# Kernel optimization log

Measured on AMD Instinct MI355X. Metric: run time of the kernel, lower is better.

Reference implementation:

```python
import jax, jax.numpy as jnp
import numpy as np

N = 100000
DEG = 16            # edges per source node (1 self-loop + 15 random)
E = N * DEG
IN_F = 128
OUT_F = 64
ALPHA = 0.2         # leaky relu negative slope


def _build_edges(key):
    # edges sorted by src (as adj.nonzero() would be), every node has >=1 out-edge
    src = jnp.repeat(jnp.arange(N, dtype=jnp.int32), DEG)
    dst = jax.random.randint(key, (E,), 0, N, dtype=jnp.int32)
    # force a self-loop as the first edge of every block
    self_pos = jnp.arange(E, dtype=jnp.int32) % DEG == 0
    dst = jnp.where(self_pos, src, dst)
    return jnp.stack([src, dst])  # [2, E]


def setup_inputs() -> dict:
    key = jax.random.key(0)
    k1, k2, k3, k4, k5, k6 = jax.random.split(key, 6)
    return {
        "input": jax.random.normal(k1, (N, IN_F), dtype=jnp.float32),
        "edge": _build_edges(k2),
        "W_high": jax.random.normal(k3, (IN_F, OUT_F), dtype=jnp.float32) * 0.1,
        "W_low": jax.random.normal(k4, (IN_F, OUT_F), dtype=jnp.float32) * 0.1,
        "a_high": jax.random.normal(k5, (1, 2 * OUT_F), dtype=jnp.float32) * 0.1,
        "a_low": jax.random.normal(k6, (1, 2 * OUT_F), dtype=jnp.float32) * 0.1,
    }


def _relu6(x):
    return jnp.clip(x, 0.0, 6.0)


def reference(input, edge, W_high, W_low, a_high, a_low):
    n = input.shape[0]
    src, dst = edge[0], edge[1]

    h_high = input @ W_high          # [N, F]
    h_low = input @ W_low            # [N, F]

    # a.mm(cat(h[src], h[dst]).T) == (h @ a_src)[src] + (h @ a_dst)[dst]
    f = W_high.shape[1]
    s_high = (h_high @ a_high[0, :f])[src] + (h_high @ a_high[0, f:])[dst]  # [E]
    s_low = (h_low @ a_low[0, :f])[src] + (h_low @ a_low[0, f:])[dst]

    edge_e_high = jnp.exp(-jax.nn.leaky_relu(s_high, ALPHA))  # [E], > 0
    edge_e_low = jnp.exp(-jax.nn.leaky_relu(s_low, ALPHA))

    seg = lambda v: jax.ops.segment_sum(v, src, num_segments=n, indices_are_sorted=True)

    # rowsum uses RAW exp values (before relu6/dropout), matching the source
    e_high_rowsum = seg(edge_e_high)[:, None]  # [N, 1]
    e_low_rowsum = seg(edge_e_low)[:, None]

    # relu6 clamp (dropout p=0 -> identity, eval mode)
    eh = _relu6(edge_e_high)
    el = _relu6(edge_e_low)

    # m @ (h[src] +/- h[dst]) == segment_sum over src of per-edge features
    h_agg_high = seg(h_high[src] + h_high[dst])   # [N, F]
    h_agg_low = seg(h_low[src] - h_low[dst])      # [N, F]

    # spmm: out[i] = sum_{(i,j)} e_ij * h_agg[j]
    h_prime_high = seg(eh[:, None] * h_agg_high[dst]) / e_high_rowsum
    h_prime_low = seg(el[:, None] * h_agg_low[dst]) / e_low_rowsum

    h_prime = 0.5 * (h_prime_high + h_prime_low)
    return _relu6(h_prime)  # concat=True
```

## Files before the change

### kernel.cpp

```cpp
#include <hip/hip_runtime.h>

#define N_NODES 100000
#define DEG 16
#define IN_F 128
#define OUT_F 64
#define E_EDGES (N_NODES * DEG)

typedef __bf16 bf16x8 __attribute__((ext_vector_type(8)));
typedef unsigned short u16x8 __attribute__((ext_vector_type(8)));
typedef float f32x4 __attribute__((ext_vector_type(4)));
typedef unsigned int u32x4 __attribute__((ext_vector_type(4)));

union BF8 { u16x8 u; bf16x8 b; };

__device__ inline float lo_bf(unsigned int u) {
    union { unsigned int i; float f; } v; v.i = u << 16; return v.f;
}
__device__ inline float hi_bf(unsigned int u) {
    union { unsigned int i; float f; } v; v.i = u & 0xFFFF0000u; return v.f;
}
__device__ inline unsigned short f2bf(float f) {
    union { float f; unsigned int i; } v; v.f = f;
    return (unsigned short)((v.i + 0x7FFFu + ((v.i >> 16) & 1u)) >> 16);
}
__device__ inline unsigned int packbf(float a, float b) {
    return (unsigned int)f2bf(a) | ((unsigned int)f2bf(b) << 16);
}

__global__ __launch_bounds__(256) void k_gemm(
    const float* __restrict__ in, const float* __restrict__ Wh,
    const float* __restrict__ Wl, unsigned int* __restrict__ H)
{
    __shared__ __align__(16) unsigned short ldsW[2][64][136];
    __shared__ __align__(16) unsigned short ldsA[64][136];

    {
        int n  = threadIdx.x & 63;
        int kg = threadIdx.x >> 6;
        #pragma unroll
        for (int m = 0; m < 2; m++) {
            const float* W = m ? Wl : Wh;
            #pragma unroll
            for (int i = 0; i < 32; i += 2) {
                int k = kg * 32 + i;
                float a = W[k * 64 + n];
                float b = W[(k + 1) * 64 + n];
                *(unsigned int*)&ldsW[m][n][k] = packbf(a, b);
            }
        }
    }

    int row0B = blockIdx.x * 64;
    {
        const f32x4* src = (const f32x4*)(in + (size_t)row0B * IN_F);
        #pragma unroll
        for (int i = 0; i < 8; i++) {
            int cch = threadIdx.x + 256 * i;
            int row = cch >> 5;
            int kc = (cch & 31) * 4;
            int grow = row0B + row;
            f32x4 v = (grow < N_NODES) ? src[cch]
                      : *(const f32x4*)(in + (size_t)(N_NODES - 1) * IN_F + kc);
            unsigned int p0 = packbf(v[0], v[1]);
            unsigned int p1 = packbf(v[2], v[3]);
            *(unsigned int*)&ldsA[row][kc]     = p0;
            *(unsigned int*)&ldsA[row][kc + 2] = p1;
        }
    }
    __syncthreads();

    int wv = threadIdx.x >> 6;
    int lane = threadIdx.x & 63;
    int quad = lane >> 4, c = lane & 15;
    int row0 = row0B + wv * 16;

    bf16x8 afrag[4];
    #pragma unroll
    for (int kb = 0; kb < 4; kb++) {
        BF8 a;
        a.u = *(const u16x8*)&ldsA[wv * 16 + c][kb * 32 + quad * 8];
        afrag[kb] = a.b;
    }

    f32x4 acc[2][4];
    #pragma unroll
    for (int m = 0; m < 2; m++)
        #pragma unroll
        for (int t = 0; t < 4; t++) acc[m][t] = (f32x4){0, 0, 0, 0};

    #pragma unroll
    for (int kb = 0; kb < 4; kb++) {
        #pragma unroll
        for (int t = 0; t < 4; t++) {
            int n = t * 16 + c;
            BF8 bh, bl;
            bh.u = *(const u16x8*)&ldsW[0][n][kb * 32 + quad * 8];
            bl.u = *(const u16x8*)&ldsW[1][n][kb * 32 + quad * 8];
            acc[0][t] = __builtin_amdgcn_mfma_f32_16x16x32_bf16(afrag[kb], bh.b, acc[0][t], 0, 0, 0);
            acc[1][t] = __builtin_amdgcn_mfma_f32_16x16x32_bf16(afrag[kb], bl.b, acc[1][t], 0, 0, 0);
        }
    }

    #pragma unroll
    for (int r = 0; r < 4; r++) {
        int row = row0 + quad * 4 + r;
        if (row >= N_NODES) continue;
        size_t base = (size_t)row * OUT_F + c;
        #pragma unroll
        for (int t = 0; t < 4; t++)
            H[base + t * 16] = packbf(acc[0][t][r], acc[1][t][r]);
    }
}

__global__ __launch_bounds__(256) void k_agg(
    const unsigned int* __restrict__ H, const int* __restrict__ dst,
    const float* __restrict__ ah, const float* __restrict__ al,
    unsigned int* __restrict__ HAGG, f32x4* __restrict__ s)
{
    int lane = threadIdx.x & 63;
    int node = __builtin_amdgcn_readfirstlane(blockIdx.x * 4 + (threadIdx.x >> 6));
    const int* dp = dst + node * DEG;

    unsigned int hu = H[(size_t)node * 64 + lane];
    float hh = lo_bf(hu);
    float hl = hi_bf(hu);
    float sh = 16.0f * hh;
    float sl = 16.0f * hl;

    #pragma unroll
    for (int half = 0; half < 2; half++) {
        unsigned int u[8];
        #pragma unroll
        for (int t = 0; t < 8; t++) {
            int j = dp[half * 8 + t];
            u[t] = H[(size_t)j * 64 + lane];
        }
        #pragma unroll
        for (int t = 0; t < 8; t++) { sh += lo_bf(u[t]); sl -= hi_bf(u[t]); }
    }
    HAGG[(size_t)node * 64 + lane] = packbf(sh, sl);

    float ph = hh * ah[lane];
    float qh = hh * ah[64 + lane];
    float pl = hl * al[lane];
    float ql = hl * al[64 + lane];
    #pragma unroll
    for (int o = 32; o > 0; o >>= 1) {
        ph += __shfl_xor(ph, o);
        qh += __shfl_xor(qh, o);
        pl += __shfl_xor(pl, o);
        ql += __shfl_xor(ql, o);
    }
    if (lane == 0) s[node] = (f32x4){ph, qh, pl, ql};
}

__global__ __launch_bounds__(256) void k_out(
    const unsigned int* __restrict__ HAGG, const int* __restrict__ dst,
    const f32x4* __restrict__ s, float* __restrict__ out)
{
    int lane = threadIdx.x & 63;
    int node = __builtin_amdgcn_readfirstlane(blockIdx.x * 4 + (threadIdx.x >> 6));
    const int* dp = dst + node * DEG;

    int jl = dp[lane & 15];
    f32x4 si = s[node];
    f32x4 sj = s[jl];
    float xh = si.x + sj.y;
    float xl = si.z + sj.w;
    float lh = xh > 0.0f ? xh : 0.2f * xh;
    float ll = xl > 0.0f ? xl : 0.2f * xl;
    float wh = __expf(-lh);
    float wl = __expf(-ll);
    float rh = wh, rl = wl;
    #pragma unroll
    for (int o = 8; o > 0; o >>= 1) { rh += __shfl_xor(rh, o); rl += __shfl_xor(rl, o); }
    float eh = fminf(wh, 6.0f);
    float el = fminf(wl, 6.0f);

    float acc_h = 0.0f, acc_l = 0.0f;
    #pragma unroll
    for (int half = 0; half < 2; half++) {
        unsigned int u[8];
        float weh[8], wel[8];
        #pragma unroll
        for (int t = 0; t < 8; t++) {
            int j = dp[half * 8 + t];
            u[t] = HAGG[(size_t)j * 64 + lane];
        }
        #pragma unroll
        for (int t = 0; t < 8; t++) {
            weh[t] = __shfl(eh, half * 8 + t);
            wel[t] = __shfl(el, half * 8 + t);
        }
        #pragma unroll
        for (int t = 0; t < 8; t++) {
            acc_h += weh[t] * lo_bf(u[t]);
            acc_l += wel[t] * hi_bf(u[t]);
        }
    }
    float r = 0.5f * (acc_h / rh + acc_l / rl);
    r = fminf(fmaxf(r, 0.0f), 6.0f);
    out[(size_t)node * 64 + lane] = r;
}

extern "C" void kernel_launch(void* const* d_in, const int* in_sizes, int n_in,
                              void* d_out, int out_size, void* d_ws, size_t ws_size,
                              hipStream_t stream) {
    const float* input = (const float*)d_in[0];
    const int*   edge  = (const int*)d_in[1];
    const float* Wh    = (const float*)d_in[2];
    const float* Wl    = (const float*)d_in[3];
    const float* ah    = (const float*)d_in[4];
    const float* al    = (const float*)d_in[5];
    float* out = (float*)d_out;

    unsigned int* H    = (unsigned int*)d_ws;
    unsigned int* HAGG = H + (size_t)N_NODES * 64;
    f32x4* s = (f32x4*)(HAGG + (size_t)N_NODES * 64);

    const int* dstp = edge + E_EDGES;

    k_gemm<<<1563, 256, 0, stream>>>(input, Wh, Wl, H);
    k_agg<<<N_NODES / 4, 256, 0, stream>>>(H, dstp, ah, al, HAGG, s);
    k_out<<<N_NODES / 4, 256, 0, stream>>>(HAGG, dstp, s, out);
}
```

Measured before the change: 228.6 us.

## Process four nodes per wave with double-buffered neighbor gathers in agg and out

Each wave in k_agg and k_out now handles four consecutive nodes instead of one. While it reduces the current node, it prefetches the next node's 16 neighbor rows (and attention scalars) into a second register buffer, and the grid shrinks by four. The intent is to hide gather latency with more loads in flight per wave and to amortize per-wave setup such as the attention vector loads. The cost is higher register use (two buffers of 16 values), which can lower occupancy, and fewer waves for the scheduler to switch between.

```diff
diff --git a/kernel.cpp b/kernel.cpp
--- a/kernel.cpp
+++ b/kernel.cpp
@@ -118,40 +118,62 @@
     unsigned int* __restrict__ HAGG, f32x4* __restrict__ s)
 {
     int lane = threadIdx.x & 63;
-    int node = __builtin_amdgcn_readfirstlane(blockIdx.x * 4 + (threadIdx.x >> 6));
-    const int* dp = dst + node * DEG;
-
-    unsigned int hu = H[(size_t)node * 64 + lane];
-    float hh = lo_bf(hu);
-    float hl = hi_bf(hu);
-    float sh = 16.0f * hh;
-    float sl = 16.0f * hl;
-
-    #pragma unroll
-    for (int half = 0; half < 2; half++) {
-        unsigned int u[8];
-        #pragma unroll
-        for (int t = 0; t < 8; t++) {
-            int j = dp[half * 8 + t];
-            u[t] = H[(size_t)j * 64 + lane];
-        }
-        #pragma unroll
-        for (int t = 0; t < 8; t++) { sh += lo_bf(u[t]); sl -= hi_bf(u[t]); }
-    }
-    HAGG[(size_t)node * 64 + lane] = packbf(sh, sl);
-
-    float ph = hh * ah[lane];
-    float qh = hh * ah[64 + lane];
-    float pl = hl * al[lane];
-    float ql = hl * al[64 + lane];
-    #pragma unroll
-    for (int o = 32; o > 0; o >>= 1) {
-        ph += __shfl_xor(ph, o);
-        qh += __shfl_xor(qh, o);
-        pl += __shfl_xor(pl, o);
-        ql += __shfl_xor(ql, o);
-    }
-    if (lane == 0) s[node] = (f32x4){ph, qh, pl, ql};
+    int wid = threadIdx.x >> 6;
+    int node0 = __builtin_amdgcn_readfirstlane((blockIdx.x * 4 + wid) * 4);
+
+    float a0 = ah[lane], a1 = ah[64 + lane];
+    float c0 = al[lane], c1 = al[64 + lane];
+
+    unsigned int g[2][16];
+    unsigned int hu[4];
+
+    #pragma unroll
+    for (int i = 0; i < 4; i++)
+        hu[i] = H[(size_t)(node0 + i) * 64 + lane];
+    {
+        const int* dp = dst + node0 * DEG;
+        #pragma unroll
+        for (int t = 0; t < 16; t++) {
+            int j = dp[t];
+            g[0][t] = H[(size_t)j * 64 + lane];
+        }
+    }
+
+    #pragma unroll
+    for (int i = 0; i < 4; i++) {
+        const int cur = i & 1, nxt = cur ^ 1;
+        int node = node0 + i;
+
+        if (i < 3) {
+            const int* dp = dst + (node + 1) * DEG;
+            #pragma unroll
+            for (int t = 0; t < 16; t++) {
+                int j = dp[t];
+                g[nxt][t] = H[(size_t)j * 64 + lane];
+            }
+        }
+
+        float hh = lo_bf(hu[i]);
+        float hl = hi_bf(hu[i]);
+        float sh = 16.0f * hh;
+        float sl = 16.0f * hl;
+        #pragma unroll
+        for (int t = 0; t < 16; t++) { sh += lo_bf(g[cur][t]); sl -= hi_bf(g[cur][t]); }
+        HAGG[(size_t)node * 64 + lane] = packbf(sh, sl);
+
+        float ph = hh * a0;
+        float qh = hh * a1;
+        float pl = hl * c0;
+        float ql = hl * c1;
+        #pragma unroll
+        for (int o = 32; o > 0; o >>= 1) {
+            ph += __shfl_xor(ph, o);
+            qh += __shfl_xor(qh, o);
+            pl += __shfl_xor(pl, o);
+            ql += __shfl_xor(ql, o);
+        }
+        if (lane == 0) s[node] = (f32x4){ph, qh, pl, ql};
+    }
 }
 
 __global__ __launch_bounds__(256) void k_out(
@@ -159,48 +181,65 @@
     const f32x4* __restrict__ s, float* __restrict__ out)
 {
     int lane = threadIdx.x & 63;
-    int node = __builtin_amdgcn_readfirstlane(blockIdx.x * 4 + (threadIdx.x >> 6));
-    const int* dp = dst + node * DEG;
-
-    int jl = dp[lane & 15];
-    f32x4 si = s[node];
-    f32x4 sj = s[jl];
-    float xh = si.x + sj.y;
-    float xl = si.z + sj.w;
-    float lh = xh > 0.0f ? xh : 0.2f * xh;
-    float ll = xl > 0.0f ? xl : 0.2f * xl;
-    float wh = __expf(-lh);
-    float wl = __expf(-ll);
-    float rh = wh, rl = wl;
-    #pragma unroll
-    for (int o = 8; o > 0; o >>= 1) { rh += __shfl_xor(rh, o); rl += __shfl_xor(rl, o); }
-    float eh = fminf(wh, 6.0f);
-    float el = fminf(wl, 6.0f);
-
-    float acc_h = 0.0f, acc_l = 0.0f;
-    #pragma unroll
-    for (int half = 0; half < 2; half++) {
-        unsigned int u[8];
-        float weh[8], wel[8];
-        #pragma unroll
-        for (int t = 0; t < 8; t++) {
-            int j = dp[half * 8 + t];
-            u[t] = HAGG[(size_t)j * 64 + lane];
-        }
-        #pragma unroll
-        for (int t = 0; t < 8; t++) {
-            weh[t] = __shfl(eh, half * 8 + t);
-            wel[t] = __shfl(el, half * 8 + t);
-        }
-        #pragma unroll
-        for (int t = 0; t < 8; t++) {
-            acc_h += weh[t] * lo_bf(u[t]);
-            acc_l += wel[t] * hi_bf(u[t]);
-        }
-    }
-    float r = 0.5f * (acc_h / rh + acc_l / rl);
-    r = fminf(fmaxf(r, 0.0f), 6.0f);
-    out[(size_t)node * 64 + lane] = r;
+    int wid = threadIdx.x >> 6;
+    int node0 = __builtin_amdgcn_readfirstlane((blockIdx.x * 4 + wid) * 4);
+
+    unsigned int g[2][16];
+    f32x4 sjv[2];
+
+    {
+        const int* dp = dst + node0 * DEG;
+        int jl = dp[lane & 15];
+        sjv[0] = s[jl];
+        #pragma unroll
+        for (int t = 0; t < 16; t++) {
+            int j = dp[t];
+            g[0][t] = HAGG[(size_t)j * 64 + lane];
+        }
+    }
+
+    #pragma unroll
+    for (int i = 0; i < 4; i++) {
+        const int cur = i & 1, nxt = cur ^ 1;
+        int node = node0 + i;
+
+        if (i < 3) {
+            const int* dp = dst + (node + 1) * DEG;
+            int jl = dp[lane & 15];
+            sjv[nxt] = s[jl];
+            #pragma unroll
+            for (int t = 0; t < 16; t++) {
+                int j = dp[t];
+                g[nxt][t] = HAGG[(size_t)j * 64 + lane];
+            }
+        }
+
+        f32x4 si = s[node];
+        f32x4 sj = sjv[cur];
+        float xh = si.x + sj.y;
+        float xl = si.z + sj.w;
+        float lh = xh > 0.0f ? xh : 0.2f * xh;
+        float ll = xl > 0.0f ? xl : 0.2f * xl;
+        float wh = __expf(-lh);
+        float wl = __expf(-ll);
+        float rh = wh, rl = wl;
+        #pragma unroll
+        for (int o = 8; o > 0; o >>= 1) { rh += __shfl_xor(rh, o); rl += __shfl_xor(rl, o); }
+        float eh = fminf(wh, 6.0f);
+        float el = fminf(wl, 6.0f);
+
+        float acc_h = 0.0f, acc_l = 0.0f;
+        #pragma unroll
+        for (int t = 0; t < 16; t++) {
+            float weh = __shfl(eh, t);
+            float wel = __shfl(el, t);
+            acc_h += weh * lo_bf(g[cur][t]);
+            acc_l += wel * hi_bf(g[cur][t]);
+        }
+        float r = 0.5f * (acc_h / rh + acc_l / rl);
+        r = fminf(fmaxf(r, 0.0f), 6.0f);
+        out[(size_t)node * 64 + lane] = r;
+    }
 }
 
 extern "C" void kernel_launch(void* const* d_in, const int* in_sizes, int n_in,
@@ -221,6 +260,6 @@
     const int* dstp = edge + E_EDGES;
 
     k_gemm<<<1563, 256, 0, stream>>>(input, Wh, Wl, H);
-    k_agg<<<N_NODES / 4, 256, 0, stream>>>(H, dstp, ah, al, HAGG, s);
-    k_out<<<N_NODES / 4, 256, 0, stream>>>(HAGG, dstp, s, out);
-}
+    k_agg<<<N_NODES / 16, 256, 0, stream>>>(H, dstp, ah, al, HAGG, s);
+    k_out<<<N_NODES / 16, 256, 0, stream>>>(HAGG, dstp, s, out);
+}
```

Measured after the change: 233.2 us. +2.0%, slower.

## Make GEMM persistent with register prefetch of next input tile

Applied to the files above, without the earlier changes.

The GEMM kernel becomes a grid-stride persistent kernel with 768 blocks looping over 1563 row tiles. Each block loads W into LDS once and prefetches the next tile's fp32 input into registers while doing the MFMA work on the current tile. This spreads the W staging cost over more tiles and overlaps global loads with compute, at the cost of more registers and an extra barrier per tile. Only the first of the three kernels changes, so the two gather kernels still account for most of the runtime.

```diff
diff --git a/kernel.cpp b/kernel.cpp
--- a/kernel.cpp
+++ b/kernel.cpp
@@ -5,6 +5,8 @@
 #define IN_F 128
 #define OUT_F 64
 #define E_EDGES (N_NODES * DEG)
+#define TILES 1563
+#define GEMM_GRID 768
 
 typedef __bf16 bf16x8 __attribute__((ext_vector_type(8)));
 typedef unsigned short u16x8 __attribute__((ext_vector_type(8)));
@@ -50,8 +52,16 @@
         }
     }
 
-    int row0B = blockIdx.x * 64;
+    int wv = threadIdx.x >> 6;
+    int lane = threadIdx.x & 63;
+    int quad = lane >> 4, c = lane & 15;
+
+    f32x4 av[8];
+    int tile = blockIdx.x;
+    if (tile >= TILES) return;
+
     {
+        int row0B = tile * 64;
         const f32x4* src = (const f32x4*)(in + (size_t)row0B * IN_F);
         #pragma unroll
         for (int i = 0; i < 8; i++) {
@@ -59,56 +69,77 @@
             int row = cch >> 5;
             int kc = (cch & 31) * 4;
             int grow = row0B + row;
-            f32x4 v = (grow < N_NODES) ? src[cch]
-                      : *(const f32x4*)(in + (size_t)(N_NODES - 1) * IN_F + kc);
-            unsigned int p0 = packbf(v[0], v[1]);
-            unsigned int p1 = packbf(v[2], v[3]);
-            *(unsigned int*)&ldsA[row][kc]     = p0;
-            *(unsigned int*)&ldsA[row][kc + 2] = p1;
-        }
-    }
-    __syncthreads();
-
-    int wv = threadIdx.x >> 6;
-    int lane = threadIdx.x & 63;
-    int quad = lane >> 4, c = lane & 15;
-    int row0 = row0B + wv * 16;
-
-    bf16x8 afrag[4];
-    #pragma unroll
-    for (int kb = 0; kb < 4; kb++) {
-        BF8 a;
-        a.u = *(const u16x8*)&ldsA[wv * 16 + c][kb * 32 + quad * 8];
-        afrag[kb] = a.b;
-    }
-
-    f32x4 acc[2][4];
-    #pragma unroll
-    for (int m = 0; m < 2; m++)
-        #pragma unroll
-        for (int t = 0; t < 4; t++) acc[m][t] = (f32x4){0, 0, 0, 0};
-
-    #pragma unroll
-    for (int kb = 0; kb < 4; kb++) {
-        #pragma unroll
-        for (int t = 0; t < 4; t++) {
-            int n = t * 16 + c;
-            BF8 bh, bl;
-            bh.u = *(const u16x8*)&ldsW[0][n][kb * 32 + quad * 8];
-            bl.u = *(const u16x8*)&ldsW[1][n][kb * 32 + quad * 8];
-            acc[0][t] = __builtin_amdgcn_mfma_f32_16x16x32_bf16(afrag[kb], bh.b, acc[0][t], 0, 0, 0);
-            acc[1][t] = __builtin_amdgcn_mfma_f32_16x16x32_bf16(afrag[kb], bl.b, acc[1][t], 0, 0, 0);
-        }
-    }
-
-    #pragma unroll
-    for (int r = 0; r < 4; r++) {
-        int row = row0 + quad * 4 + r;
-        if (row >= N_NODES) continue;
-        size_t base = (size_t)row * OUT_F + c;
-        #pragma unroll
-        for (int t = 0; t < 4; t++)
-            H[base + t * 16] = packbf(acc[0][t][r], acc[1][t][r]);
+            av[i] = (grow < N_NODES) ? src[cch]
+                    : *(const f32x4*)(in + (size_t)(N_NODES - 1) * IN_F + kc);
+        }
+    }
+
+    for (; tile < TILES; tile += GEMM_GRID) {
+        int row0B = tile * 64;
+
+        __syncthreads();
+        #pragma unroll
+        for (int i = 0; i < 8; i++) {
+            int cch = threadIdx.x + 256 * i;
+            int row = cch >> 5;
+            int kc = (cch & 31) * 4;
+            *(unsigned int*)&ldsA[row][kc]     = packbf(av[i][0], av[i][1]);
+            *(unsigned int*)&ldsA[row][kc + 2] = packbf(av[i][2], av[i][3]);
+        }
+        __syncthreads();
+
+        int ntile = tile + GEMM_GRID;
+        if (ntile < TILES) {
+            int nrow0 = ntile * 64;
+            const f32x4* src = (const f32x4*)(in + (size_t)nrow0 * IN_F);
+            #pragma unroll
+            for (int i = 0; i < 8; i++) {
+                int cch = threadIdx.x + 256 * i;
+                int row = cch >> 5;
+                int kc = (cch & 31) * 4;
+                int grow = nrow0 + row;
+                av[i] = (grow < N_NODES) ? src[cch]
+                        : *(const f32x4*)(in + (size_t)(N_NODES - 1) * IN_F + kc);
+            }
+        }
+
+        bf16x8 afrag[4];
+        #pragma unroll
+        for (int kb = 0; kb < 4; kb++) {
+            BF8 a;
+            a.u = *(const u16x8*)&ldsA[wv * 16 + c][kb * 32 + quad * 8];
+            afrag[kb] = a.b;
+        }
+
+        f32x4 acc[2][4];
+        #pragma unroll
+        for (int m = 0; m < 2; m++)
+            #pragma unroll
+            for (int t = 0; t < 4; t++) acc[m][t] = (f32x4){0, 0, 0, 0};
+
+        #pragma unroll
+        for (int kb = 0; kb < 4; kb++) {
+            #pragma unroll
+            for (int t = 0; t < 4; t++) {
+                int n = t * 16 + c;
+                BF8 bh, bl;
+                bh.u = *(const u16x8*)&ldsW[0][n][kb * 32 + quad * 8];
+                bl.u = *(const u16x8*)&ldsW[1][n][kb * 32 + quad * 8];
+                acc[0][t] = __builtin_amdgcn_mfma_f32_16x16x32_bf16(afrag[kb], bh.b, acc[0][t], 0, 0, 0);
+                acc[1][t] = __builtin_amdgcn_mfma_f32_16x16x32_bf16(afrag[kb], bl.b, acc[1][t], 0, 0, 0);
+            }
+        }
+
+        int row0 = row0B + wv * 16;
+        #pragma unroll
+        for (int r = 0; r < 4; r++) {
+            int row = row0 + quad * 4 + r;
+            if (row >= N_NODES) continue;
+            size_t base = (size_t)row * OUT_F + c;
+            #pragma unroll
+            for (int t = 0; t < 4; t++)
+                H[base + t * 16] = packbf(acc[0][t][r], acc[1][t][r]);
+        }
     }
 }
 
@@ -220,7 +251,7 @@
 
     const int* dstp = edge + E_EDGES;
 
-    k_gemm<<<1563, 256, 0, stream>>>(input, Wh, Wl, H);
+    k_gemm<<<GEMM_GRID, 256, 0, stream>>>(input, Wh, Wl, H);
     k_agg<<<N_NODES / 4, 256, 0, stream>>>(H, dstp, ah, al, HAGG, s);
     k_out<<<N_NODES / 4, 256, 0, stream>>>(HAGG, dstp, s, out);
 }
```

After: 225.8 us. No clear change (-1.2%).
